# Optimization experiments

Hardware: AMD Instinct MI355X
Metric: run time of the kernel (lower is better)

## Reference

```python
import jax, jax.numpy as jnp
import numpy as np

HILBERT_BITS = 8
NDIM = 3


def hilbert_distance(grid, bits=HILBERT_BITS):
    """Vectorized Skilling transform: grid [..., 3] int32 in [0, 2**bits-1] -> Hilbert index [...] int32.
    Exact port of hilbertcurve.HilbertCurve.distance_from_point (n=3, p=bits)."""
    x = [grid[..., i] for i in range(NDIM)]
    m = 1 << (bits - 1)
    # Inverse undo excess work
    q = m
    while q > 1:
        pm = q - 1
        for i in range(NDIM):
            cond = (x[i] & q) != 0
            if i == 0:
                x[0] = jnp.where(cond, x[0] ^ pm, x[0])
            else:
                t = (x[0] ^ x[i]) & pm
                x0n = jnp.where(cond, x[0] ^ pm, x[0] ^ t)
                xin = jnp.where(cond, x[i], x[i] ^ t)
                x[0], x[i] = x0n, xin
        q >>= 1
    # Gray encode
    x[1] = x[1] ^ x[0]
    x[2] = x[2] ^ x[1]
    t = jnp.zeros_like(x[2])
    q = m
    while q > 1:
        t = jnp.where((x[2] & q) != 0, t ^ (q - 1), t)
        q >>= 1
    x = [xi ^ t for xi in x]
    # Interleave bits, MSB first, dim order 0,1,2 -> h has bits*3 bits (24 fits int32)
    h = jnp.zeros_like(x[0])
    for bpos in range(bits - 1, -1, -1):
        for i in range(NDIM):
            h = (h << 1) | ((x[i] >> bpos) & 1)
    return h


def hilbert_orders(x, bits=HILBERT_BITS):
    # x: [B, N, 3] float. Per-batch min/max normalization, then quantize to grid.
    mins = x.min(axis=1, keepdims=True)
    maxs = x.max(axis=1, keepdims=True)
    span = jnp.maximum(maxs - mins, 1e-6)
    norm = (x - mins) / span
    mx = (1 << bits) - 1
    grid_h = jnp.clip(norm * mx, 0, mx).astype(jnp.int32)
    grid_t = jnp.clip(norm[..., ::-1] * mx, 0, mx).astype(jnp.int32)  # [z,y,x] variant
    order_h = jnp.argsort(hilbert_distance(grid_h, bits), axis=-1)
    order_t = jnp.argsort(hilbert_distance(grid_t, bits), axis=-1)
    return order_h, order_t


def setup_inputs() -> dict:
    key = jax.random.key(0)
    k1, k2, k3 = jax.random.split(key, 3)
    B, N, D = 16, 4096, 384
    x = jax.random.normal(k1, (B, N, 3), dtype=jnp.float32)
    W = jax.random.normal(k2, (D, 3), dtype=jnp.float32) * 0.5
    b = jax.random.normal(k3, (D,), dtype=jnp.float32) * 0.1
    gamma = jnp.ones((2, D), dtype=jnp.float32)
    beta = jnp.zeros((2, D), dtype=jnp.float32)
    return {"x": x, "W": W, "b": b, "gamma": gamma, "beta": beta}


def reference(x, W, b, gamma, beta):
    order_h, order_t = hilbert_orders(x)                     # [B, N] each
    pts_h = jnp.take_along_axis(x, order_h[..., None], axis=1)  # [B, N, 3]
    pts_t = jnp.take_along_axis(x, order_t[..., None], axis=1)
    base_h = jnp.einsum('bnc,dc->bnd', pts_h, W) + b         # Linear(3, D)
    base_t = jnp.einsum('bnc,dc->bnd', pts_t, W) + b
    tokens_h = base_h * gamma[0] + beta[0]
    tokens_t = base_t * gamma[1] + beta[1]
    return jnp.concatenate([tokens_h, tokens_t], axis=1)     # [B, 2N, D]
```

## Files before the change

### kernel.cpp

```cpp
#include <hip/hip_runtime.h>
#include <stdint.h>

#define BATCH 16
#define NPTS 4096
#define DIM 384
#define NTOK (2*NPTS)
#define F4PT (DIM/4)

typedef unsigned long long u64;

__device__ __forceinline__ uint32_t spread3(uint32_t x) {
    x = (x | (x << 8)) & 0x00F00Fu;
    x = (x | (x << 4)) & 0x0C30C3u;
    x = (x | (x << 2)) & 0x249249u;
    return x;
}

__device__ __forceinline__ uint32_t hilbert3(uint32_t x0, uint32_t x1, uint32_t x2) {
    #pragma unroll
    for (uint32_t q = 128; q > 1; q >>= 1) {
        uint32_t pm = q - 1;
        if (x0 & q) x0 ^= pm;
        uint32_t t = (x0 ^ x1) & pm;
        if (x1 & q) { x0 ^= pm; } else { x0 ^= t; x1 ^= t; }
        t = (x0 ^ x2) & pm;
        if (x2 & q) { x0 ^= pm; } else { x0 ^= t; x2 ^= t; }
    }
    x1 ^= x0;
    x2 ^= x1;
    uint32_t t = 0;
    #pragma unroll
    for (uint32_t q = 128; q > 1; q >>= 1) { if (x2 & q) t ^= (q - 1); }
    x0 ^= t; x1 ^= t; x2 ^= t;
    return (spread3(x0) << 2) | (spread3(x1) << 1) | spread3(x2);
}

__global__ __launch_bounds__(512) void order_radix_o(const float* __restrict__ x,
                                                     u64* __restrict__ kws) {
    const int bi = blockIdx.x;
    const int b = bi >> 4;
    const int v = (bi >> 3) & 1;
    const int oct = bi & 7;
    const int t = threadIdx.x;
    const int lane = t & 63;
    const int w = t >> 6;

    __shared__ u64 skey[512];
    __shared__ uint32_t hist[6 * 128];
    __shared__ uint32_t baseArr[16];
    __shared__ float red[8 * 6];

    const float* xb = x + (size_t)b * NPTS * 3;
    const float4* xb4 = (const float4*)xb;

    float mnx = 1e30f, mny = 1e30f, mnz = 1e30f;
    float mxx = -1e30f, mxy = -1e30f, mxz = -1e30f;
    #pragma unroll
    for (int h = 0; h < 2; ++h) {
        float4 q0 = xb4[h * 1536 + 3 * t + 0];
        float4 q1 = xb4[h * 1536 + 3 * t + 1];
        float4 q2 = xb4[h * 1536 + 3 * t + 2];
        float px[4] = {q0.x, q0.w, q1.z, q2.y};
        float py[4] = {q0.y, q1.x, q1.w, q2.z};
        float pz[4] = {q0.z, q1.y, q2.x, q2.w};
        #pragma unroll
        for (int r = 0; r < 4; ++r) {
            mnx = fminf(mnx, px[r]); mxx = fmaxf(mxx, px[r]);
            mny = fminf(mny, py[r]); mxy = fmaxf(mxy, py[r]);
            mnz = fminf(mnz, pz[r]); mxz = fmaxf(mxz, pz[r]);
        }
    }
    #pragma unroll
    for (int off = 32; off > 0; off >>= 1) {
        mnx = fminf(mnx, __shfl_xor(mnx, off));
        mny = fminf(mny, __shfl_xor(mny, off));
        mnz = fminf(mnz, __shfl_xor(mnz, off));
        mxx = fmaxf(mxx, __shfl_xor(mxx, off));
        mxy = fmaxf(mxy, __shfl_xor(mxy, off));
        mxz = fmaxf(mxz, __shfl_xor(mxz, off));
    }
    if (lane == 0) {
        red[w*6+0] = mnx; red[w*6+1] = mny; red[w*6+2] = mnz;
        red[w*6+3] = mxx; red[w*6+4] = mxy; red[w*6+5] = mxz;
    }
    hist[t] = 0u;
    if (t < 256) hist[512 + t] = 0u;
    __syncthreads();
    if (t == 0) {
        for (int ww = 1; ww < 8; ++ww) {
            mnx = fminf(mnx, red[ww*6+0]); mny = fminf(mny, red[ww*6+1]);
            mnz = fminf(mnz, red[ww*6+2]); mxx = fmaxf(mxx, red[ww*6+3]);
            mxy = fmaxf(mxy, red[ww*6+4]); mxz = fmaxf(mxz, red[ww*6+5]);
        }
        red[0] = mnx; red[1] = mny; red[2] = mnz;
        red[3] = fmaxf(mxx - mnx, 1e-6f);
        red[4] = fmaxf(mxy - mny, 1e-6f);
        red[5] = fmaxf(mxz - mnz, 1e-6f);
    }
    __syncthreads();
    mnx = red[0]; mny = red[1]; mnz = red[2];
    const float spx = red[3], spy = red[4], spz = red[5];

    u64 key;
    {
        const int n0 = (oct << 9) + t;
        float cx = xb[3*n0+0], cy = xb[3*n0+1], cz = xb[3*n0+2];
        float gx = fminf(fmaxf(((cx - mnx) / spx) * 255.0f, 0.0f), 255.0f);
        float gy = fminf(fmaxf(((cy - mny) / spy) * 255.0f, 0.0f), 255.0f);
        float gz = fminf(fmaxf(((cz - mnz) / spz) * 255.0f, 0.0f), 255.0f);
        uint32_t ix = (uint32_t)(int)gx;
        uint32_t iy = (uint32_t)(int)gy;
        uint32_t iz = (uint32_t)(int)gz;
        uint32_t a0 = v ? iz : ix;
        uint32_t a2 = v ? ix : iz;
        uint32_t code = hilbert3(a0, iy, a2);
        key = ((u64)code << 12) | (u64)n0;
    }

    const u64 below_mask = (1ull << lane) - 1ull;
    u64* segk = kws + (((b << 1) | v) << 12);

    #pragma unroll
    for (int p = 0; p < 6; ++p) {
        const int sh = 12 + 4 * p;
        uint32_t* histp = hist + p * 128;

        unsigned d = (unsigned)(key >> sh) & 15u;
        u64 m = ~0ull;
        #pragma unroll
        for (int bit = 0; bit < 4; ++bit) {
            u64 bal = __ballot((int)((d >> bit) & 1u));
            m &= ((d >> bit) & 1u) ? bal : ~bal;
        }
        unsigned rk = (unsigned)__popcll(m & below_mask);
        if (rk == 0u)
            histp[d * 8 + w] = (unsigned)__popcll(m);
        __syncthreads();

        if (t < 16) {
            unsigned running = 0;
            #pragma unroll
            for (int s = 0; s < 8; ++s) {
                unsigned hv = histp[t * 8 + s];
                histp[t * 8 + s] = running;
                running += hv;
            }
            unsigned tv = running;
            #pragma unroll
            for (int off = 1; off < 16; off <<= 1) {
                unsigned nv = __shfl_up(tv, off);
                if (lane >= off) tv += nv;
            }
            baseArr[t] = tv - running;
        }
        __syncthreads();

        unsigned pos = baseArr[d] + histp[d * 8 + w] + rk;

        if (p < 5) {
            skey[pos] = key;
            __syncthreads();
            key = skey[t];
        } else {
            segk[(oct << 9) + pos] = key;
        }
    }
}

__global__ __launch_bounds__(512) void order_merge_o(const u64* __restrict__ kws,
                                                     int* __restrict__ order) {
    const int bi = blockIdx.x;
    const int b = bi >> 4;
    const int v = (bi >> 3) & 1;
    const int oct = bi & 7;
    const int t = threadIdx.x;

    __shared__ u64 sk[7 * 512];

    const u64* segk = kws + (((b << 1) | v) << 12);
    u64 k = segk[(oct << 9) + t];

    #pragma unroll
    for (int j = 0; j < 7; ++j) {
        int oq = j + (j >= oct ? 1 : 0);
        sk[j * 512 + t] = segk[(oq << 9) + t];
    }
    __syncthreads();

    int rank = t;
    #pragma unroll
    for (int j = 0; j < 7; ++j) {
        const u64* s = &sk[j * 512];
        int c = 0;
        #pragma unroll
        for (int step = 512; step >= 1; step >>= 1) {
            if (c + step <= 512 && s[c + step - 1] < k) c += step;
        }
        rank += c;
    }

    order[(((b << 1) | v) << 12) + rank] = (int)(k & 0xFFFull);
}

__global__ __launch_bounds__(256) void token_kernel(const float* __restrict__ x,
                                                    const float* __restrict__ W,
                                                    const float* __restrict__ bias,
                                                    const float* __restrict__ gamma,
                                                    const float* __restrict__ beta,
                                                    const int* __restrict__ order,
                                                    float* __restrict__ out) {
    __shared__ __align__(16) float sW0[2][DIM];
    __shared__ __align__(16) float sW1[2][DIM];
    __shared__ __align__(16) float sW2[2][DIM];
    __shared__ __align__(16) float sC[2][DIM];
    for (int i = threadIdx.x; i < 2 * DIM; i += 256) {
        int v = i / DIM;
        int d = i - v * DIM;
        float g = gamma[i];
        sW0[v][d] = g * W[d*3+0];
        sW1[v][d] = g * W[d*3+1];
        sW2[v][d] = g * W[d*3+2];
        sC[v][d]  = g * bias[d] + beta[i];
    }
    __syncthreads();

    const int total = BATCH * NTOK * F4PT;
    const int stride = gridDim.x * blockDim.x;
    for (int g4 = blockIdx.x * blockDim.x + threadIdx.x; g4 < total; g4 += stride) {
        int token = g4 / F4PT;
        int grp = g4 - token * F4PT;
        int b = token >> 13;
        int nn = token & (NTOK - 1);
        int v = nn >> 12;
        int n = nn & (NPTS - 1);
        int idx = order[(((b << 1) | v) << 12) + n];
        const float* p = x + (size_t)(b * NPTS + idx) * 3;
        float px = p[0], py = p[1], pz = p[2];
        int d0 = grp << 2;
        float4 w0 = *(const float4*)&sW0[v][d0];
        float4 w1 = *(const float4*)&sW1[v][d0];
        float4 w2 = *(const float4*)&sW2[v][d0];
        float4 c  = *(const float4*)&sC[v][d0];
        float4 o;
        o.x = px*w0.x + py*w1.x + pz*w2.x + c.x;
        o.y = px*w0.y + py*w1.y + pz*w2.y + c.y;
        o.z = px*w0.z + py*w1.z + pz*w2.z + c.z;
        o.w = px*w0.w + py*w1.w + pz*w2.w + c.w;
        reinterpret_cast<float4*>(out)[g4] = o;
    }
}

extern "C" void kernel_launch(void* const* d_in, const int* in_sizes, int n_in,
                              void* d_out, int out_size, void* d_ws, size_t ws_size,
                              hipStream_t stream) {
    const float* x     = (const float*)d_in[0];
    const float* W     = (const float*)d_in[1];
    const float* bias  = (const float*)d_in[2];
    const float* gamma = (const float*)d_in[3];
    const float* beta  = (const float*)d_in[4];

    u64* kws   = (u64*)d_ws;
    int* order = (int*)(kws + 32 * 4096);

    hipLaunchKernelGGL(order_radix_o, dim3(BATCH * 16), dim3(512), 0, stream, x, kws);
    hipLaunchKernelGGL(order_merge_o, dim3(BATCH * 16), dim3(512), 0, stream, kws, order);
    hipLaunchKernelGGL(token_kernel,  dim3(2048),       dim3(256), 0, stream,
                       x, W, bias, gamma, beta, order, (float*)d_out);
}
```

Measured before the change: 53.90 us.

## Fuse merge-rank and token emission into one kernel, scattering rows by rank

```diff
diff --git a/kernel.cpp b/kernel.cpp
--- a/kernel.cpp
+++ b/kernel.cpp
@@ -167,86 +167,81 @@
     }
 }
 
-__global__ __launch_bounds__(512) void order_merge_o(const u64* __restrict__ kws,
-                                                     int* __restrict__ order) {
+__global__ __launch_bounds__(512) void merge_emit_kernel(const float* __restrict__ x,
+                                                         const float* __restrict__ W,
+                                                         const float* __restrict__ bias,
+                                                         const float* __restrict__ gamma,
+                                                         const float* __restrict__ beta,
+                                                         const u64* __restrict__ kws,
+                                                         float4* __restrict__ out4) {
     const int bi = blockIdx.x;
     const int b = bi >> 4;
     const int v = (bi >> 3) & 1;
     const int oct = bi & 7;
     const int t = threadIdx.x;
 
-    __shared__ u64 sk[7 * 512];
+    __shared__ u64 runs[8 * 512];
+    __shared__ __align__(16) float sw0[DIM], sw1[DIM], sw2[DIM], sc[DIM];
+    __shared__ float cxs[512], cys[512], czs[512];
+    __shared__ int rnk[512];
+
+    if (t < DIM) {
+        float g = gamma[v * DIM + t];
+        sw0[t] = g * W[t*3+0];
+        sw1[t] = g * W[t*3+1];
+        sw2[t] = g * W[t*3+2];
+        sc[t]  = g * bias[t] + beta[v * DIM + t];
+    }
 
     const u64* segk = kws + (((b << 1) | v) << 12);
-    u64 k = segk[(oct << 9) + t];
-
+    #pragma unroll
+    for (int j = 0; j < 8; ++j)
+        runs[(j << 9) + t] = segk[(j << 9) + t];
+    __syncthreads();
+
+    u64 k = runs[(oct << 9) + t];
+    int base7[7], c[7];
     #pragma unroll
     for (int j = 0; j < 7; ++j) {
-        int oq = j + (j >= oct ? 1 : 0);
-        sk[j * 512 + t] = segk[(oq << 9) + t];
-    }
-    __syncthreads();
-
+        base7[j] = (j + (j >= oct ? 1 : 0)) << 9;
+        c[j] = 0;
+    }
+    #pragma unroll
+    for (int step = 512; step >= 1; step >>= 1) {
+        #pragma unroll
+        for (int j = 0; j < 7; ++j) {
+            if (c[j] + step <= 512 && runs[base7[j] + c[j] + step - 1] < k)
+                c[j] += step;
+        }
+    }
     int rank = t;
     #pragma unroll
-    for (int j = 0; j < 7; ++j) {
-        const u64* s = &sk[j * 512];
-        int c = 0;
-        #pragma unroll
-        for (int step = 512; step >= 1; step >>= 1) {
-            if (c + step <= 512 && s[c + step - 1] < k) c += step;
-        }
-        rank += c;
-    }
-
-    order[(((b << 1) | v) << 12) + rank] = (int)(k & 0xFFFull);
-}
-
-__global__ __launch_bounds__(256) void token_kernel(const float* __restrict__ x,
-                                                    const float* __restrict__ W,
-                                                    const float* __restrict__ bias,
-                                                    const float* __restrict__ gamma,
-                                                    const float* __restrict__ beta,
-                                                    const int* __restrict__ order,
-                                                    float* __restrict__ out) {
-    __shared__ __align__(16) float sW0[2][DIM];
-    __shared__ __align__(16) float sW1[2][DIM];
-    __shared__ __align__(16) float sW2[2][DIM];
-    __shared__ __align__(16) float sC[2][DIM];
-    for (int i = threadIdx.x; i < 2 * DIM; i += 256) {
-        int v = i / DIM;
-        int d = i - v * DIM;
-        float g = gamma[i];
-        sW0[v][d] = g * W[d*3+0];
-        sW1[v][d] = g * W[d*3+1];
-        sW2[v][d] = g * W[d*3+2];
-        sC[v][d]  = g * bias[d] + beta[i];
-    }
-    __syncthreads();
-
-    const int total = BATCH * NTOK * F4PT;
-    const int stride = gridDim.x * blockDim.x;
-    for (int g4 = blockIdx.x * blockDim.x + threadIdx.x; g4 < total; g4 += stride) {
-        int token = g4 / F4PT;
-        int grp = g4 - token * F4PT;
-        int b = token >> 13;
-        int nn = token & (NTOK - 1);
-        int v = nn >> 12;
-        int n = nn & (NPTS - 1);
-        int idx = order[(((b << 1) | v) << 12) + n];
-        const float* p = x + (size_t)(b * NPTS + idx) * 3;
-        float px = p[0], py = p[1], pz = p[2];
-        int d0 = grp << 2;
-        float4 w0 = *(const float4*)&sW0[v][d0];
-        float4 w1 = *(const float4*)&sW1[v][d0];
-        float4 w2 = *(const float4*)&sW2[v][d0];
-        float4 c  = *(const float4*)&sC[v][d0];
+    for (int j = 0; j < 7; ++j) rank += c[j];
+
+    {
+        int idx = (int)(k & 0xFFFull);
+        const float* p = x + (size_t)b * NPTS * 3 + idx * 3;
+        cxs[t] = p[0]; cys[t] = p[1]; czs[t] = p[2];
+        rnk[t] = rank;
+    }
+    __syncthreads();
+
+    const int tokbase = (b << 13) + (v << 12);
+    for (int i = t; i < 512 * F4PT; i += 512) {
+        int r = i / F4PT;
+        int g = i - r * F4PT;
+        float pxr = cxs[r], pyr = cys[r], pzr = czs[r];
+        int d0 = g << 2;
+        float4 w0 = *(const float4*)&sw0[d0];
+        float4 w1 = *(const float4*)&sw1[d0];
+        float4 w2 = *(const float4*)&sw2[d0];
+        float4 cc = *(const float4*)&sc[d0];
         float4 o;
-        o.x = px*w0.x + py*w1.x + pz*w2.x + c.x;
-        o.y = px*w0.y + py*w1.y + pz*w2.y + c.y;
-        o.z = px*w0.z + py*w1.z + pz*w2.z + c.z;
-        o.w = px*w0.w + py*w1.w + pz*w2.w + c.w;
-        reinterpret_cast<float4*>(out)[g4] = o;
+        o.x = pxr*w0.x + pyr*w1.x + pzr*w2.x + cc.x;
+        o.y = pxr*w0.y + pyr*w1.y + pzr*w2.y + cc.y;
+        o.z = pxr*w0.z + pyr*w1.z + pzr*w2.z + cc.z;
+        o.w = pxr*w0.w + pyr*w1.w + pzr*w2.w + cc.w;
+        out4[(size_t)(tokbase + rnk[r]) * F4PT + g] = o;
     }
 }
 
@@ -259,11 +254,9 @@
     const float* gamma = (const float*)d_in[3];
     const float* beta  = (const float*)d_in[4];
 
-    u64* kws   = (u64*)d_ws;
-    int* order = (int*)(kws + 32 * 4096);
-
-    hipLaunchKernelGGL(order_radix_o, dim3(BATCH * 16), dim3(512), 0, stream, x, kws);
-    hipLaunchKernelGGL(order_merge_o, dim3(BATCH * 16), dim3(512), 0, stream, kws, order);
-    hipLaunchKernelGGL(token_kernel,  dim3(2048),       dim3(256), 0, stream,
-                       x, W, bias, gamma, beta, order, (float*)d_out);
-}
+    u64* kws = (u64*)d_ws;
+
+    hipLaunchKernelGGL(order_radix_o,     dim3(BATCH * 16), dim3(512), 0, stream, x, kws);
+    hipLaunchKernelGGL(merge_emit_kernel, dim3(BATCH * 16), dim3(512), 0, stream,
+                       x, W, bias, gamma, beta, kws, (float4*)d_out);
+}
```

Result: faster. 50.78 us (-5.8%).
